# Kernel optimization log

Hardware: AMD Instinct MI355X
Metric: run time of the kernel (lower is better)

## Reference

```python
import jax, jax.numpy as jnp
import numpy as np

B, T, S, H = 16, 1024, 2048, 1024


def setup_inputs() -> dict:
    key = jax.random.key(0)
    k1, k2, k3, k4, k5 = jax.random.split(key, 5)
    output = jax.random.normal(k1, (B, T, H), dtype=jnp.float32)
    context = jax.random.normal(k2, (B, S, H), dtype=jnp.float32)
    # nn.Linear(H, H, bias=False): weight [H, H], y = x @ W.T
    attn_weight = jax.random.normal(k3, (H, H), dtype=jnp.float32) * (1.0 / np.sqrt(H))
    # nn.Linear(2H, H): weight [H, 2H], bias [H]
    linear_out_w = jax.random.normal(k4, (H, 2 * H), dtype=jnp.float32) * (1.0 / np.sqrt(2 * H))
    linear_out_b = jax.random.normal(k5, (H,), dtype=jnp.float32) * 0.01
    return {"output": output, "context": context, "attn_weight": attn_weight,
            "linear_out_w": linear_out_w, "linear_out_b": linear_out_b}


def reference(output, context, attn_weight, linear_out_w, linear_out_b):
    # weighted query projection (use_weight=True)
    q = jnp.einsum('bth,oh->bto', output, attn_weight)  # [B,T,H]
    # scores + softmax over encoder positions
    attn = jax.nn.softmax(jnp.einsum('bth,bsh->bts', q, context), axis=-1)  # [B,T,S]
    mix = jnp.einsum('bts,bsh->bth', attn, context)  # [B,T,H]
    comb = jnp.concatenate([mix, q], axis=-1)  # [B,T,2H]
    out = jnp.tanh(jnp.einsum('btk,hk->bth', comb, linear_out_w) + linear_out_b)
    return (out, attn)
```

## Files before the change

kernel.cpp:

```cpp
#include <hip/hip_runtime.h>
#include <math.h>

typedef short bf16x8 __attribute__((ext_vector_type(8)));
typedef float f32x4 __attribute__((ext_vector_type(4)));
typedef unsigned short u16;

#define AS1 __attribute__((address_space(1)))
#define AS3 __attribute__((address_space(3)))

constexpr int kB = 16, kT = 1024, kS = 2048, kH = 1024;
constexpr long NTH = (long)kB * kT * kH;
constexpr long NSH = (long)kB * kS * kH;

__device__ __forceinline__ u16 bf16_rne(float x) {
    unsigned u = __float_as_uint(x);
    u += 0x7FFFu + ((u >> 16) & 1u);
    return (u16)(u >> 16);
}
__device__ __forceinline__ float bf16_f32(u16 h) {
    return __uint_as_float(((unsigned)h) << 16);
}
__device__ __forceinline__ void split2(float x, u16& hi, u16& lo) {
    hi = bf16_rne(x);
    lo = bf16_rne(x - bf16_f32(hi));
}


__device__ __forceinline__ void stage_mat(const u16* __restrict__ g, long ld,
                                          u16* lds, int t, int wave) {
#pragma unroll
    for (int c = 0; c < 4; ++c) {
        int u = c * 512 + t;
        int r = u >> 3, j = u & 7;
        const u16* src = g + (long)r * ld + ((j ^ (r & 7)) << 3);
        u16* dst = lds + c * 4096 + wave * 512;
        __builtin_amdgcn_global_load_lds((AS1 void*)src, (AS3 void*)dst, 16, 0, 0);
    }
}

__device__ __forceinline__ void tile_compute(const u16* As, const u16* Bs,
                                             f32x4 acc[8][4], int wr, int wc,
                                             int l15, int cbu0, int cbu1) {
    bf16x8 b[4][2];
#pragma unroll
    for (int j = 0; j < 4; ++j) {
        const u16* base = Bs + (wc * 64 + j * 16 + l15) * 64;
        b[j][0] = *(const bf16x8*)(base + cbu0);
        b[j][1] = *(const bf16x8*)(base + cbu1);
    }
#pragma unroll
    for (int qm = 0; qm < 2; ++qm) {
        bf16x8 a[4][2];
#pragma unroll
        for (int i = 0; i < 4; ++i) {
            const u16* base = As + (wr * 128 + qm * 64 + i * 16 + l15) * 64;
            a[i][0] = *(const bf16x8*)(base + cbu0);
            a[i][1] = *(const bf16x8*)(base + cbu1);
        }
        __builtin_amdgcn_s_setprio(1);
#pragma unroll
        for (int i = 0; i < 4; ++i)
#pragma unroll
            for (int j = 0; j < 4; ++j) {
                acc[qm * 4 + i][j] = __builtin_amdgcn_mfma_f32_16x16x32_bf16(
                    a[i][0], b[j][0], acc[qm * 4 + i][j], 0, 0, 0);
                acc[qm * 4 + i][j] = __builtin_amdgcn_mfma_f32_16x16x32_bf16(
                    a[i][1], b[j][1], acc[qm * 4 + i][j], 0, 0, 0);
            }
        __builtin_amdgcn_s_setprio(0);
    }
}

#define WAIT_VM(N)                                            \
    asm volatile("s_waitcnt vmcnt(" #N ")" ::: "memory");     \
    __builtin_amdgcn_s_barrier();                             \
    __builtin_amdgcn_sched_barrier(0);

#define POST_BARRIER()                                        \
    __builtin_amdgcn_sched_barrier(0);                        \
    __builtin_amdgcn_s_barrier();                             \
    __builtin_amdgcn_sched_barrier(0);

template <int NT, int TPS>
__device__ __forceinline__ void gemm_core(const u16* a0, const u16* a1, const u16* a2,
                                          long lda,
                                          const u16* b0, const u16* b1, const u16* b2,
                                          long ldb, f32x4 acc[8][4]) {
    __shared__ u16 As[2][256 * 64], Bs[2][256 * 64];
    const int t = threadIdx.x, lane = t & 63, wave = t >> 6;
    const int wr = wave >> 2, wc = wave & 3, l15 = lane & 15, quad = lane >> 4;
    const int swzb = (l15 & 7) << 4;
    const int cbu0 = ((quad * 16) ^ swzb) >> 1;
    const int cbu1 = ((quad * 16 + 64) ^ swzb) >> 1;

    auto srcA = [&](int kt) {
        int seg = kt / TPS;
        const u16* p = (seg == 0) ? a0 : (seg == 1 ? a1 : a2);
        return p + (long)(kt % TPS) * 64;
    };
    auto srcB = [&](int kt) {
        int seg = kt / TPS;
        const u16* p = (seg == 0) ? b0 : (seg == 1 ? b1 : b2);
        return p + (long)(kt % TPS) * 64;
    };

    stage_mat(srcA(0), lda, As[0], t, wave);
    stage_mat(srcB(0), ldb, Bs[0], t, wave);
    __builtin_amdgcn_sched_barrier(0);
    stage_mat(srcA(1), lda, As[1], t, wave);
    stage_mat(srcB(1), ldb, Bs[1], t, wave);
    __builtin_amdgcn_sched_barrier(0);

#pragma unroll 1
    for (int it = 0; it < NT / 2 - 1; ++it) {
        int kt = 2 * it;
        WAIT_VM(8)
        tile_compute(As[0], Bs[0], acc, wr, wc, l15, cbu0, cbu1);
        POST_BARRIER()
        stage_mat(srcA(kt + 2), lda, As[0], t, wave);
        stage_mat(srcB(kt + 2), ldb, Bs[0], t, wave);

        WAIT_VM(8)
        tile_compute(As[1], Bs[1], acc, wr, wc, l15, cbu0, cbu1);
        POST_BARRIER()
        stage_mat(srcA(kt + 3), lda, As[1], t, wave);
        stage_mat(srcB(kt + 3), ldb, Bs[1], t, wave);
    }
    WAIT_VM(8)
    tile_compute(As[0], Bs[0], acc, wr, wc, l15, cbu0, cbu1);
    WAIT_VM(0)
    tile_compute(As[1], Bs[1], acc, wr, wc, l15, cbu0, cbu1);
}

__global__ __launch_bounds__(512, 2) void k_gemm_q(const u16* __restrict__ oh,
                                                   const u16* __restrict__ ol,
                                                   const u16* __restrict__ awh,
                                                   const u16* __restrict__ awl,
                                                   u16* __restrict__ Qhi,
                                                   u16* __restrict__ Qlo) {
    const long bm = (long)blockIdx.y * 256, bn = (long)blockIdx.x * 256;
    f32x4 acc[8][4] = {};
    gemm_core<48, 16>(oh + bm * kH, ol + bm * kH, oh + bm * kH, kH,
                      awh + bn * kH, awh + bn * kH, awl + bn * kH, kH, acc);
    const int t = threadIdx.x, lane = t & 63, wave = t >> 6;
    const int wr = wave >> 2, wc = wave & 3, l15 = lane & 15, quad = lane >> 4;
#pragma unroll
    for (int i = 0; i < 8; ++i)
#pragma unroll
        for (int j = 0; j < 4; ++j)
#pragma unroll
            for (int r = 0; r < 4; ++r) {
                long m = bm + wr * 128 + i * 16 + quad * 4 + r;
                long n = bn + wc * 64 + j * 16 + l15;
                float v = acc[i][j][r];
                u16 h = bf16_rne(v);
                Qhi[m * kH + n] = h;
                Qlo[m * kH + n] = bf16_rne(v - bf16_f32(h));
            }
}

__global__ __launch_bounds__(512, 2) void k_gemm_logits(const u16* __restrict__ Qh,
                                                        const u16* __restrict__ Ql,
                                                        const u16* __restrict__ Ch,
                                                        const u16* __restrict__ Cl,
                                                        float* __restrict__ Cout) {
    const int l = blockIdx.x;
    const int xcd = l & 7, slot = l >> 3;
    const int z = xcd + ((slot >> 5) << 3);
    const int inner = slot & 31;
    const long bn = (long)(inner & 7) * 256;
    const long bm = (long)(inner >> 3) * 256;
    const u16* qh = Qh + (long)z * kT * kH + bm * kH;
    const u16* ql = Ql + (long)z * kT * kH + bm * kH;
    const u16* ch = Ch + (long)z * kS * kH + bn * kH;
    const u16* cl = Cl + (long)z * kS * kH + bn * kH;
    f32x4 acc[8][4] = {};
    gemm_core<48, 16>(qh, ql, qh, kH, ch, ch, cl, kH, acc);
    float* C = Cout + (long)z * kT * kS;
    const int t = threadIdx.x, lane = t & 63, wave = t >> 6;
    const int wr = wave >> 2, wc = wave & 3, l15 = lane & 15, quad = lane >> 4;
#pragma unroll
    for (int i = 0; i < 8; ++i)
#pragma unroll
        for (int j = 0; j < 4; ++j)
#pragma unroll
            for (int r = 0; r < 4; ++r) {
                long m = bm + wr * 128 + i * 16 + quad * 4 + r;
                long n = bn + wc * 64 + j * 16 + l15;
                C[m * kS + n] = acc[i][j][r];
            }
}

__global__ __launch_bounds__(512, 2) void k_gemm_mix(const u16* __restrict__ attnb,
                                                     const u16* __restrict__ ctxT,
                                                     u16* __restrict__ Mixb) {
    const int l = blockIdx.x;
    const int xcd = l & 7, slot = l >> 3;
    const int z = xcd + ((slot >> 4) << 3);
    const int inner = slot & 15;
    const long bn = (long)(inner & 3) * 256;
    const long bm = (long)(inner >> 2) * 256;
    const u16* Ab = attnb + (long)z * kT * kS + bm * kS;
    const u16* Bb = ctxT + (long)z * kH * kS + bn * kS;
    f32x4 acc[8][4] = {};
    gemm_core<32, 32>(Ab, Ab, Ab, kS, Bb, Bb, Bb, kS, acc);
    u16* C = Mixb + (long)z * kT * kH;
    const int t = threadIdx.x, lane = t & 63, wave = t >> 6;
    const int wr = wave >> 2, wc = wave & 3, l15 = lane & 15, quad = lane >> 4;
#pragma unroll
    for (int i = 0; i < 8; ++i)
#pragma unroll
        for (int j = 0; j < 4; ++j)
#pragma unroll
            for (int r = 0; r < 4; ++r) {
                long m = bm + wr * 128 + i * 16 + quad * 4 + r;
                long n = bn + wc * 64 + j * 16 + l15;
                C[m * kH + n] = bf16_rne(acc[i][j][r]);
            }
}

__global__ __launch_bounds__(512, 2) void k_gemm_out(const u16* __restrict__ mixc,
                                                     const u16* __restrict__ qc,
                                                     const u16* __restrict__ lwb,
                                                     const float* __restrict__ bias,
                                                     float* __restrict__ Out) {
    const long bm = (long)blockIdx.y * 256, bn = (long)blockIdx.x * 256;
    f32x4 acc[8][4] = {};
    gemm_core<32, 16>(mixc + bm * kH, qc + bm * kH, qc + bm * kH, kH,
                      lwb + bn * 2 * kH, lwb + bn * 2 * kH + kH, lwb + bn * 2 * kH + kH,
                      2 * kH, acc);
    const int t = threadIdx.x, lane = t & 63, wave = t >> 6;
    const int wr = wave >> 2, wc = wave & 3, l15 = lane & 15, quad = lane >> 4;
#pragma unroll
    for (int j = 0; j < 4; ++j) {
        long n = bn + wc * 64 + j * 16 + l15;
        float bj = bias[n];
#pragma unroll
        for (int i = 0; i < 8; ++i)
#pragma unroll
            for (int r = 0; r < 4; ++r) {
                long m = bm + wr * 128 + i * 16 + quad * 4 + r;
                Out[m * kH + n] = tanhf(acc[i][j][r] + bj);
            }
    }
}

__global__ __launch_bounds__(256) void split_f32(const float* __restrict__ src,
                                                 u16* __restrict__ hi, u16* __restrict__ lo,
                                                 long n4) {
    for (long i = (long)blockIdx.x * 256 + threadIdx.x; i < n4; i += (long)gridDim.x * 256) {
        float4 v = ((const float4*)src)[i];
        u16 h0, l0, h1, l1, h2, l2, h3, l3;
        split2(v.x, h0, l0); split2(v.y, h1, l1);
        split2(v.z, h2, l2); split2(v.w, h3, l3);
        ((ushort4*)hi)[i] = make_ushort4(h0, h1, h2, h3);
        ((ushort4*)lo)[i] = make_ushort4(l0, l1, l2, l3);
    }
}

__global__ __launch_bounds__(256) void cvt_f32(const float* __restrict__ src,
                                               u16* __restrict__ dst, long n4) {
    for (long i = (long)blockIdx.x * 256 + threadIdx.x; i < n4; i += (long)gridDim.x * 256) {
        float4 v = ((const float4*)src)[i];
        ((ushort4*)dst)[i] = make_ushort4(bf16_rne(v.x), bf16_rne(v.y),
                                          bf16_rne(v.z), bf16_rne(v.w));
    }
}

__global__ __launch_bounds__(256) void copy16(const uint4* __restrict__ src,
                                              uint4* __restrict__ dst, long n) {
    for (long i = (long)blockIdx.x * 256 + threadIdx.x; i < n; i += (long)gridDim.x * 256)
        dst[i] = src[i];
}

__global__ __launch_bounds__(256) void transpose_bf16(const u16* __restrict__ in,
                                                      u16* __restrict__ outp) {
    __shared__ u16 tile[64 * 72];
    const int t = threadIdx.x;
    const u16* src = in + (long)blockIdx.z * kS * kH + (long)(blockIdx.y * 64) * kH
                     + blockIdx.x * 64;
#pragma unroll
    for (int it = 0; it < 2; ++it) {
        int idx = it * 256 + t;
        int s = idx >> 3, hc = (idx & 7) << 3;
        uint4 v = *(const uint4*)(src + (long)s * kH + hc);
        const u16* pv = (const u16*)&v;
#pragma unroll
        for (int k = 0; k < 8; ++k) tile[(hc + k) * 72 + s] = pv[k];
    }
    __syncthreads();
    u16* dst = outp + (long)blockIdx.z * kH * kS + (long)(blockIdx.x * 64) * kS
               + blockIdx.y * 64;
#pragma unroll
    for (int it = 0; it < 2; ++it) {
        int idx = it * 256 + t;
        int h = idx >> 3, sc = (idx & 7) << 3;
        *(uint4*)(dst + (long)h * kS + sc) = *(const uint4*)&tile[h * 72 + sc];
    }
}

__global__ __launch_bounds__(256) void softmax_rows(float* __restrict__ P,
                                                    u16* __restrict__ Pb) {
    __shared__ float red[4];
    float* p = P + (long)blockIdx.x * kS;
    u16* pb = Pb + (long)blockIdx.x * kS;
    const int t = threadIdx.x;

    float4 v0 = ((const float4*)p)[t];
    float4 v1 = ((const float4*)p)[t + 256];

    float m = fmaxf(fmaxf(fmaxf(v0.x, v0.y), fmaxf(v0.z, v0.w)),
                    fmaxf(fmaxf(v1.x, v1.y), fmaxf(v1.z, v1.w)));
#pragma unroll
    for (int o = 32; o > 0; o >>= 1) m = fmaxf(m, __shfl_xor(m, o));
    if ((t & 63) == 0) red[t >> 6] = m;
    __syncthreads();
    m = fmaxf(fmaxf(red[0], red[1]), fmaxf(red[2], red[3]));
    __syncthreads();

    v0.x = expf(v0.x - m); v0.y = expf(v0.y - m);
    v0.z = expf(v0.z - m); v0.w = expf(v0.w - m);
    v1.x = expf(v1.x - m); v1.y = expf(v1.y - m);
    v1.z = expf(v1.z - m); v1.w = expf(v1.w - m);

    float s = v0.x + v0.y + v0.z + v0.w + v1.x + v1.y + v1.z + v1.w;
#pragma unroll
    for (int o = 32; o > 0; o >>= 1) s += __shfl_xor(s, o);
    if ((t & 63) == 0) red[t >> 6] = s;
    __syncthreads();
    s = red[0] + red[1] + red[2] + red[3];

    const float inv = 1.0f / s;
    v0.x *= inv; v0.y *= inv; v0.z *= inv; v0.w *= inv;
    v1.x *= inv; v1.y *= inv; v1.z *= inv; v1.w *= inv;

    ((float4*)p)[t]       = v0;
    ((float4*)p)[t + 256] = v1;
    ((ushort4*)pb)[t]       = make_ushort4(bf16_rne(v0.x), bf16_rne(v0.y),
                                           bf16_rne(v0.z), bf16_rne(v0.w));
    ((ushort4*)pb)[t + 256] = make_ushort4(bf16_rne(v1.x), bf16_rne(v1.y),
                                           bf16_rne(v1.z), bf16_rne(v1.w));
}

extern "C" void kernel_launch(void* const* d_in, const int* in_sizes, int n_in,
                              void* d_out, int out_size, void* d_ws, size_t ws_size,
                              hipStream_t stream) {
    (void)in_sizes; (void)n_in; (void)out_size; (void)ws_size;

    const float* outp = (const float*)d_in[0];
    const float* ctx  = (const float*)d_in[1];
    const float* aw   = (const float*)d_in[2];
    const float* lw   = (const float*)d_in[3];
    const float* lb   = (const float*)d_in[4];

    float* out  = (float*)d_out;
    float* attn = out + NTH;

    u16* ws = (u16*)d_ws;
    u16* ctx_hi = ws;
    u16* ctx_lo = ws + NSH;
    u16* q_hi = (u16*)out;
    u16* q_lo = q_hi + NTH;
    u16* oh  = (u16*)attn;
    u16* ol  = oh + NTH;
    u16* awh = ol + NTH;
    u16* awl = awh + (long)kH * kH;
    u16* ctxT  = ws + NSH;
    u16* attnb = ws;
    u16* mixb  = q_lo;
    u16* q_c   = ws;
    u16* mix_c = ws + NTH;
    u16* lwb   = ws + 2 * NTH;

    split_f32<<<2048, 256, 0, stream>>>(ctx, ctx_hi, ctx_lo, NSH / 4);
    split_f32<<<2048, 256, 0, stream>>>(outp, oh, ol, NTH / 4);
    split_f32<<<1024, 256, 0, stream>>>(aw, awh, awl, (long)kH * kH / 4);

    k_gemm_q<<<dim3(kH / 256, (kB * kT) / 256), 512, 0, stream>>>(oh, ol, awh, awl,
                                                                  q_hi, q_lo);
    k_gemm_logits<<<512, 512, 0, stream>>>(q_hi, q_lo, ctx_hi, ctx_lo, attn);

    transpose_bf16<<<dim3(kH / 64, kS / 64, kB), 256, 0, stream>>>(ctx_hi, ctxT);
    softmax_rows<<<kB * kT, 256, 0, stream>>>(attn, attnb);

    k_gemm_mix<<<256, 512, 0, stream>>>(attnb, ctxT, mixb);

    copy16<<<2048, 256, 0, stream>>>((const uint4*)q_hi, (uint4*)ws, (2 * NTH) / 8);
    cvt_f32<<<2048, 256, 0, stream>>>(lw, lwb, (long)kH * 2 * kH / 4);

    k_gemm_out<<<dim3(kH / 256, (kB * kT) / 256), 512, 0, stream>>>(mix_c, q_c, lwb, lb, out);
}
```

Baseline: 891.3 us.

## Restructure GEMM main loop into four-phase interleaved load/MFMA schedule

Replaces the two-stage double-buffered GEMM loop with a four-phase schedule per K tile. Each phase issues half-tile global-to-LDS loads for the next A tile or for the B tile two steps ahead, then runs a 16-MFMA quadrant under raised priority, with barriers between phases. The aim is to spread memory traffic across the compute and keep the matrix units busier than whole-tile staging followed by bulk compute allows. It adds more barriers per tile and clamped, redundant loads past the last tile.

```diff
diff --git a/kernel.cpp b/kernel.cpp
--- a/kernel.cpp
+++ b/kernel.cpp
@@ -26,60 +26,17 @@
 }
 
 
-__device__ __forceinline__ void stage_mat(const u16* __restrict__ g, long ld,
-                                          u16* lds, int t, int wave) {
-#pragma unroll
-    for (int c = 0; c < 4; ++c) {
-        int u = c * 512 + t;
-        int r = u >> 3, j = u & 7;
-        const u16* src = g + (long)r * ld + ((j ^ (r & 7)) << 3);
-        u16* dst = lds + c * 4096 + wave * 512;
-        __builtin_amdgcn_global_load_lds((AS1 void*)src, (AS3 void*)dst, 16, 0, 0);
-    }
-}
-
-__device__ __forceinline__ void tile_compute(const u16* As, const u16* Bs,
-                                             f32x4 acc[8][4], int wr, int wc,
-                                             int l15, int cbu0, int cbu1) {
-    bf16x8 b[4][2];
-#pragma unroll
-    for (int j = 0; j < 4; ++j) {
-        const u16* base = Bs + (wc * 64 + j * 16 + l15) * 64;
-        b[j][0] = *(const bf16x8*)(base + cbu0);
-        b[j][1] = *(const bf16x8*)(base + cbu1);
-    }
-#pragma unroll
-    for (int qm = 0; qm < 2; ++qm) {
-        bf16x8 a[4][2];
-#pragma unroll
-        for (int i = 0; i < 4; ++i) {
-            const u16* base = As + (wr * 128 + qm * 64 + i * 16 + l15) * 64;
-            a[i][0] = *(const bf16x8*)(base + cbu0);
-            a[i][1] = *(const bf16x8*)(base + cbu1);
-        }
-        __builtin_amdgcn_s_setprio(1);
-#pragma unroll
-        for (int i = 0; i < 4; ++i)
-#pragma unroll
-            for (int j = 0; j < 4; ++j) {
-                acc[qm * 4 + i][j] = __builtin_amdgcn_mfma_f32_16x16x32_bf16(
-                    a[i][0], b[j][0], acc[qm * 4 + i][j], 0, 0, 0);
-                acc[qm * 4 + i][j] = __builtin_amdgcn_mfma_f32_16x16x32_bf16(
-                    a[i][1], b[j][1], acc[qm * 4 + i][j], 0, 0, 0);
-            }
-        __builtin_amdgcn_s_setprio(0);
-    }
-}
-
-#define WAIT_VM(N)                                            \
-    asm volatile("s_waitcnt vmcnt(" #N ")" ::: "memory");     \
-    __builtin_amdgcn_s_barrier();                             \
-    __builtin_amdgcn_sched_barrier(0);
-
-#define POST_BARRIER()                                        \
-    __builtin_amdgcn_sched_barrier(0);                        \
-    __builtin_amdgcn_s_barrier();                             \
-    __builtin_amdgcn_sched_barrier(0);
+#define PHASE_PRE()                                          \
+    __builtin_amdgcn_sched_barrier(0);                       \
+    __builtin_amdgcn_s_barrier();                            \
+    asm volatile("s_waitcnt lgkmcnt(0)" ::: "memory");       \
+    __builtin_amdgcn_sched_barrier(0);                       \
+    __builtin_amdgcn_s_setprio(1);
+
+#define PHASE_POST()                                         \
+    __builtin_amdgcn_s_setprio(0);                           \
+    __builtin_amdgcn_sched_barrier(0);                       \
+    __builtin_amdgcn_s_barrier();
 
 template <int NT, int TPS>
 __device__ __forceinline__ void gemm_core(const u16* a0, const u16* a1, const u16* a2,
@@ -103,33 +60,107 @@
         const u16* p = (seg == 0) ? b0 : (seg == 1 ? b1 : b2);
         return p + (long)(kt % TPS) * 64;
     };
-
-    stage_mat(srcA(0), lda, As[0], t, wave);
-    stage_mat(srcB(0), ldb, Bs[0], t, wave);
-    __builtin_amdgcn_sched_barrier(0);
-    stage_mat(srcA(1), lda, As[1], t, wave);
-    stage_mat(srcB(1), ldb, Bs[1], t, wave);
-    __builtin_amdgcn_sched_barrier(0);
+    auto stageA = [&](int kt, int h, int buf) {
+        const u16* g = srcA(kt < NT ? kt : NT - 1) + (long)h * 128 * lda;
+        u16* region = &As[buf][h * 8192];
+#pragma unroll
+        for (int c = 0; c < 2; ++c) {
+            int u = c * 512 + t;
+            int r = u >> 3, j8 = u & 7;
+            const u16* src = g + (long)r * lda + ((j8 ^ (r & 7)) << 3);
+            u16* dst = region + c * 4096 + wave * 512;
+            __builtin_amdgcn_global_load_lds((AS1 void*)src, (AS3 void*)dst, 16, 0, 0);
+        }
+    };
+    auto stageB = [&](int kt, int h, int buf) {
+        const u16* g = srcB(kt < NT ? kt : NT - 1) + (long)h * 128 * ldb;
+        u16* region = &Bs[buf][h * 8192];
+#pragma unroll
+        for (int c = 0; c < 2; ++c) {
+            int u = c * 512 + t;
+            int r = u >> 3, j8 = u & 7;
+            const u16* src = g + (long)r * ldb + ((j8 ^ (r & 7)) << 3);
+            u16* dst = region + c * 4096 + wave * 512;
+            __builtin_amdgcn_global_load_lds((AS1 void*)src, (AS3 void*)dst, 16, 0, 0);
+        }
+    };
+
+    stageB(0, 0, 0); __builtin_amdgcn_sched_barrier(0);
+    stageB(0, 1, 0); __builtin_amdgcn_sched_barrier(0);
+    stageA(0, 0, 0); __builtin_amdgcn_sched_barrier(0);
+    stageA(0, 1, 0); __builtin_amdgcn_sched_barrier(0);
+    stageB(1, 0, 1); __builtin_amdgcn_sched_barrier(0);
+    stageB(1, 1, 1); __builtin_amdgcn_sched_barrier(0);
+    asm volatile("s_waitcnt vmcnt(4)" ::: "memory");
+    __builtin_amdgcn_s_barrier();
 
 #pragma unroll 1
-    for (int it = 0; it < NT / 2 - 1; ++it) {
-        int kt = 2 * it;
-        WAIT_VM(8)
-        tile_compute(As[0], Bs[0], acc, wr, wc, l15, cbu0, cbu1);
-        POST_BARRIER()
-        stage_mat(srcA(kt + 2), lda, As[0], t, wave);
-        stage_mat(srcB(kt + 2), ldb, Bs[0], t, wave);
-
-        WAIT_VM(8)
-        tile_compute(As[1], Bs[1], acc, wr, wc, l15, cbu0, cbu1);
-        POST_BARRIER()
-        stage_mat(srcA(kt + 3), lda, As[1], t, wave);
-        stage_mat(srcB(kt + 3), ldb, Bs[1], t, wave);
-    }
-    WAIT_VM(8)
-    tile_compute(As[0], Bs[0], acc, wr, wc, l15, cbu0, cbu1);
-    WAIT_VM(0)
-    tile_compute(As[1], Bs[1], acc, wr, wc, l15, cbu0, cbu1);
+    for (int j = 0; j < NT; ++j) {
+        const int c = j & 1;
+        bf16x8 a[4][2], bA[2][2], bB[2][2];
+
+        auto mfma16 = [&](bf16x8 (&a4)[4][2], bf16x8 (&b2)[2][2], int ih, int jh) {
+#pragma unroll
+            for (int i2 = 0; i2 < 4; ++i2)
+#pragma unroll
+                for (int j2 = 0; j2 < 2; ++j2) {
+                    acc[ih * 4 + i2][jh * 2 + j2] = __builtin_amdgcn_mfma_f32_16x16x32_bf16(
+                        a4[i2][0], b2[j2][0], acc[ih * 4 + i2][jh * 2 + j2], 0, 0, 0);
+                    acc[ih * 4 + i2][jh * 2 + j2] = __builtin_amdgcn_mfma_f32_16x16x32_bf16(
+                        a4[i2][1], b2[j2][1], acc[ih * 4 + i2][jh * 2 + j2], 0, 0, 0);
+                }
+        };
+
+#pragma unroll
+        for (int i = 0; i < 4; ++i) {
+            const u16* base = &As[c][(wr * 128 + i * 16 + l15) * 64];
+            a[i][0] = *(const bf16x8*)(base + cbu0);
+            a[i][1] = *(const bf16x8*)(base + cbu1);
+        }
+#pragma unroll
+        for (int jj = 0; jj < 2; ++jj) {
+            const u16* base = &Bs[c][(wc * 64 + jj * 16 + l15) * 64];
+            bA[jj][0] = *(const bf16x8*)(base + cbu0);
+            bA[jj][1] = *(const bf16x8*)(base + cbu1);
+        }
+        stageA(j + 1, 0, c ^ 1);
+        PHASE_PRE()
+        mfma16(a, bA, 0, 0);
+        PHASE_POST()
+
+#pragma unroll
+        for (int jj = 0; jj < 2; ++jj) {
+            const u16* base = &Bs[c][(wc * 64 + (2 + jj) * 16 + l15) * 64];
+            bB[jj][0] = *(const bf16x8*)(base + cbu0);
+            bB[jj][1] = *(const bf16x8*)(base + cbu1);
+        }
+        stageA(j + 1, 1, c ^ 1);
+        PHASE_PRE()
+        mfma16(a, bB, 0, 1);
+        PHASE_POST()
+
+#pragma unroll
+        for (int i = 0; i < 4; ++i) {
+            const u16* base = &As[c][(wr * 128 + (4 + i) * 16 + l15) * 64];
+            a[i][0] = *(const bf16x8*)(base + cbu0);
+            a[i][1] = *(const bf16x8*)(base + cbu1);
+        }
+        stageB(j + 2, 0, c);
+        PHASE_PRE()
+        mfma16(a, bA, 1, 0);
+        PHASE_POST()
+
+        stageB(j + 2, 1, c);
+        __builtin_amdgcn_sched_barrier(0);
+        __builtin_amdgcn_s_barrier();
+        __builtin_amdgcn_s_setprio(1);
+        mfma16(a, bB, 1, 1);
+        __builtin_amdgcn_s_setprio(0);
+        __builtin_amdgcn_sched_barrier(0);
+        asm volatile("s_waitcnt vmcnt(4)" ::: "memory");
+        __builtin_amdgcn_s_barrier();
+    }
+    asm volatile("s_waitcnt vmcnt(0)" ::: "memory");
 }
 
 __global__ __launch_bounds__(512, 2) void k_gemm_q(const u16* __restrict__ oh,
```

Measured after the change: 980.5 us. +10.0%, slower.

## Add K-split half-tile pipelined GEMM core for the logits kernel

Applied to the files above, without the earlier changes.

Adds a new GEMM mainloop that stages each 64-wide K tile as two 32-wide halves into double-buffered LDS. Each half gets its own vmcnt wait and barrier, and the next tile's half is loaded while the current half is computed. MFMA issue is bracketed with setprio. Only the logits GEMM uses it. The aim is finer-grained overlap of global-to-LDS loads with MFMA compute, at the cost of twice as many barriers per tile and a different LDS swizzle.

```diff
diff --git a/kernel.cpp b/kernel.cpp
--- a/kernel.cpp
+++ b/kernel.cpp
@@ -24,7 +24,6 @@
     hi = bf16_rne(x);
     lo = bf16_rne(x - bf16_f32(hi));
 }
-
 
 __device__ __forceinline__ void stage_mat(const u16* __restrict__ g, long ld,
                                           u16* lds, int t, int wave) {
@@ -130,6 +129,76 @@
     tile_compute(As[0], Bs[0], acc, wr, wc, l15, cbu0, cbu1);
     WAIT_VM(0)
     tile_compute(As[1], Bs[1], acc, wr, wc, l15, cbu0, cbu1);
+}
+
+template <int NT, int TPS>
+__device__ __forceinline__ void gemm_core_ks(const u16* a0, const u16* a1, const u16* a2,
+                                             long lda,
+                                             const u16* b0, const u16* b1, const u16* b2,
+                                             long ldb, f32x4 acc[8][4]) {
+    __shared__ u16 As[2][2][256 * 32], Bs[2][2][256 * 32];
+    const int t = threadIdx.x, lane = t & 63, wave = t >> 6;
+    const int wr = wave >> 2, wc = wave & 3, l15 = lane & 15, quad = lane >> 4;
+    const int cu = (quad ^ ((l15 >> 1) & 3)) << 3;
+
+    auto srcA = [&](int kt) {
+        int seg = kt / TPS;
+        const u16* p = (seg == 0) ? a0 : (seg == 1 ? a1 : a2);
+        return p + (long)(kt % TPS) * 64;
+    };
+    auto srcB = [&](int kt) {
+        int seg = kt / TPS;
+        const u16* p = (seg == 0) ? b0 : (seg == 1 ? b1 : b2);
+        return p + (long)(kt % TPS) * 64;
+    };
+    auto stageH = [&](const u16* g, long ld, int kh, u16* region) {
+        const u16* gh = g + kh * 32;
+#pragma unroll
+        for (int c = 0; c < 2; ++c) {
+            int u = c * 512 + t;
+            int r = u >> 2, c16 = u & 3;
+            const u16* src = gh + (long)r * ld + ((c16 ^ ((r >> 1) & 3)) << 3);
+            u16* dst = region + c * 4096 + wave * 512;
+            __builtin_amdgcn_global_load_lds((AS1 void*)src, (AS3 void*)dst, 16, 0, 0);
+        }
+    };
+
+    stageH(srcA(0), lda, 0, As[0][0]);
+    stageH(srcB(0), ldb, 0, Bs[0][0]);
+    __builtin_amdgcn_sched_barrier(0);
+    stageH(srcA(0), lda, 1, As[0][1]);
+    stageH(srcB(0), ldb, 1, Bs[0][1]);
+    __builtin_amdgcn_sched_barrier(0);
+
+#pragma unroll 1
+    for (int j = 0; j < NT; ++j) {
+        const int buf = j & 1;
+        const int skt = (j + 1 < NT) ? j + 1 : NT - 1;
+#pragma unroll
+        for (int kh = 0; kh < 2; ++kh) {
+            asm volatile("s_waitcnt vmcnt(4)" ::: "memory");
+            __builtin_amdgcn_s_barrier();
+            __builtin_amdgcn_sched_barrier(0);
+            stageH(srcA(skt), lda, kh, As[buf ^ 1][kh]);
+            stageH(srcB(skt), ldb, kh, Bs[buf ^ 1][kh]);
+            bf16x8 a[8], b[4];
+#pragma unroll
+            for (int i = 0; i < 8; ++i)
+                a[i] = *(const bf16x8*)(&As[buf][kh][(wr * 128 + i * 16 + l15) * 32 + cu]);
+#pragma unroll
+            for (int jj = 0; jj < 4; ++jj)
+                b[jj] = *(const bf16x8*)(&Bs[buf][kh][(wc * 64 + jj * 16 + l15) * 32 + cu]);
+            __builtin_amdgcn_s_setprio(1);
+#pragma unroll
+            for (int i = 0; i < 8; ++i)
+#pragma unroll
+                for (int jj = 0; jj < 4; ++jj)
+                    acc[i][jj] = __builtin_amdgcn_mfma_f32_16x16x32_bf16(
+                        a[i], b[jj], acc[i][jj], 0, 0, 0);
+            __builtin_amdgcn_s_setprio(0);
+        }
+    }
+    asm volatile("s_waitcnt vmcnt(0)" ::: "memory");
 }
 
 __global__ __launch_bounds__(512, 2) void k_gemm_q(const u16* __restrict__ oh,
@@ -175,7 +244,7 @@
     const u16* ch = Ch + (long)z * kS * kH + bn * kH;
     const u16* cl = Cl + (long)z * kS * kH + bn * kH;
     f32x4 acc[8][4] = {};
-    gemm_core<48, 16>(qh, ql, qh, kH, ch, ch, cl, kH, acc);
+    gemm_core_ks<48, 16>(qh, ql, qh, kH, ch, ch, cl, kH, acc);
     float* C = Cout + (long)z * kT * kS;
     const int t = threadIdx.x, lane = t & 63, wave = t >> 6;
     const int wr = wave >> 2, wc = wave & 3, l15 = lane & 15, quad = lane >> 4;
```

Measured after the change: 925.1 us. 3.8% more time.

## Use four-phase interleaved load/MFMA pipeline for logits GEMM

Applied to the files above, without the earlier changes.

Adds a new GEMM core for the logits kernel that splits each K-tile into four MFMA phases. Half-tile global-to-LDS loads are interleaved between the phases, with barriers and setprio around each MFMA cluster. It stages B two tiles ahead and A one tile ahead, so memory traffic overlaps with compute more finely than the old two-buffer loop. The cost is more barriers per tile and more complex buffer-reuse ordering, which could introduce races or stalls.

```diff
diff --git a/kernel.cpp b/kernel.cpp
--- a/kernel.cpp
+++ b/kernel.cpp
@@ -24,7 +24,6 @@
     hi = bf16_rne(x);
     lo = bf16_rne(x - bf16_f32(hi));
 }
-
 
 __device__ __forceinline__ void stage_mat(const u16* __restrict__ g, long ld,
                                           u16* lds, int t, int wave) {
@@ -130,6 +129,148 @@
     tile_compute(As[0], Bs[0], acc, wr, wc, l15, cbu0, cbu1);
     WAIT_VM(0)
     tile_compute(As[1], Bs[1], acc, wr, wc, l15, cbu0, cbu1);
+}
+
+template <int NT, int TPS>
+__device__ __forceinline__ void gemm_core_p4(const u16* a0p, const u16* a1p,
+                                             const u16* a2p, long lda,
+                                             const u16* b0p, const u16* b1p,
+                                             const u16* b2p, long ldb, f32x4 acc[8][4]) {
+    __shared__ u16 As[2][256 * 64], Bs[2][256 * 64];
+    const int t = threadIdx.x, lane = t & 63, wave = t >> 6;
+    const int wr = wave >> 2, wc = wave & 3, l15 = lane & 15, quad = lane >> 4;
+    const int swzb = (l15 & 7) << 4;
+    const int cbu0 = ((quad * 16) ^ swzb) >> 1;
+    const int cbu1 = ((quad * 16 + 64) ^ swzb) >> 1;
+
+    auto srcA = [&](int kt) {
+        int seg = kt / TPS;
+        const u16* p = (seg == 0) ? a0p : (seg == 1 ? a1p : a2p);
+        return p + (long)(kt % TPS) * 64;
+    };
+    auto srcB = [&](int kt) {
+        int seg = kt / TPS;
+        const u16* p = (seg == 0) ? b0p : (seg == 1 ? b1p : b2p);
+        return p + (long)(kt % TPS) * 64;
+    };
+    auto stageH = [&](const u16* g, long ld, int h, u16* bufbase) {
+        const u16* gh = g + (long)h * 128 * ld;
+        u16* region = bufbase + h * 8192;
+#pragma unroll
+        for (int cc = 0; cc < 2; ++cc) {
+            int u = cc * 512 + t;
+            int r = u >> 3, j8 = u & 7;
+            const u16* src = gh + (long)r * ld + ((j8 ^ (r & 7)) << 3);
+            u16* dst = region + cc * 4096 + wave * 512;
+            __builtin_amdgcn_global_load_lds((AS1 void*)src, (AS3 void*)dst, 16, 0, 0);
+        }
+    };
+
+    stageH(srcA(0), lda, 0, As[0]);
+    stageH(srcA(0), lda, 1, As[0]);
+    stageH(srcB(0), ldb, 0, Bs[0]);
+    stageH(srcB(0), ldb, 1, Bs[0]);
+    stageH(srcB(1), ldb, 0, Bs[1]);
+    stageH(srcB(1), ldb, 1, Bs[1]);
+    asm volatile("s_waitcnt vmcnt(4)" ::: "memory");
+    __builtin_amdgcn_s_barrier();
+
+#pragma unroll 1
+    for (int j = 0; j < NT; ++j) {
+        const int c = j & 1;
+        const int jA = (j + 1 < NT) ? j + 1 : NT - 1;
+        const int jB = (j + 2 < NT) ? j + 2 : NT - 1;
+        const u16* As_c = As[c];
+        const u16* Bs_c = Bs[c];
+        bf16x8 aF[8][2], bF[4][2];
+
+#pragma unroll
+        for (int n = 0; n < 4; ++n) {
+            const u16* base = Bs_c + (wc * 64 + n * 16 + l15) * 64;
+            bF[n][0] = *(const bf16x8*)(base + cbu0);
+            bF[n][1] = *(const bf16x8*)(base + cbu1);
+        }
+#pragma unroll
+        for (int i = 0; i < 4; ++i) {
+            const u16* base = As_c + (wr * 128 + i * 16 + l15) * 64;
+            aF[i][0] = *(const bf16x8*)(base + cbu0);
+            aF[i][1] = *(const bf16x8*)(base + cbu1);
+        }
+        stageH(srcA(jA), lda, 0, As[c ^ 1]);
+        __builtin_amdgcn_s_barrier();
+        asm volatile("s_waitcnt lgkmcnt(0)" ::: "memory");
+        __builtin_amdgcn_sched_barrier(0);
+        __builtin_amdgcn_s_setprio(1);
+#pragma unroll
+        for (int i = 0; i < 4; ++i)
+#pragma unroll
+            for (int n = 0; n < 2; ++n) {
+                acc[i][n] = __builtin_amdgcn_mfma_f32_16x16x32_bf16(
+                    aF[i][0], bF[n][0], acc[i][n], 0, 0, 0);
+                acc[i][n] = __builtin_amdgcn_mfma_f32_16x16x32_bf16(
+                    aF[i][1], bF[n][1], acc[i][n], 0, 0, 0);
+            }
+        __builtin_amdgcn_s_setprio(0);
+        __builtin_amdgcn_sched_barrier(0);
+        __builtin_amdgcn_s_barrier();
+
+#pragma unroll
+        for (int i = 0; i < 4; ++i) {
+            const u16* base = As_c + (wr * 128 + 64 + i * 16 + l15) * 64;
+            aF[4 + i][0] = *(const bf16x8*)(base + cbu0);
+            aF[4 + i][1] = *(const bf16x8*)(base + cbu1);
+        }
+        stageH(srcA(jA), lda, 1, As[c ^ 1]);
+        __builtin_amdgcn_s_barrier();
+        asm volatile("s_waitcnt lgkmcnt(0)" ::: "memory");
+        __builtin_amdgcn_sched_barrier(0);
+        __builtin_amdgcn_s_setprio(1);
+#pragma unroll
+        for (int i = 0; i < 4; ++i)
+#pragma unroll
+            for (int n = 0; n < 2; ++n) {
+                acc[i][2 + n] = __builtin_amdgcn_mfma_f32_16x16x32_bf16(
+                    aF[i][0], bF[2 + n][0], acc[i][2 + n], 0, 0, 0);
+                acc[i][2 + n] = __builtin_amdgcn_mfma_f32_16x16x32_bf16(
+                    aF[i][1], bF[2 + n][1], acc[i][2 + n], 0, 0, 0);
+            }
+        __builtin_amdgcn_s_setprio(0);
+        __builtin_amdgcn_sched_barrier(0);
+        __builtin_amdgcn_s_barrier();
+
+        stageH(srcB(jB), ldb, 0, Bs[c]);
+        __builtin_amdgcn_s_barrier();
+        __builtin_amdgcn_s_setprio(1);
+#pragma unroll
+        for (int i = 0; i < 4; ++i)
+#pragma unroll
+            for (int n = 0; n < 2; ++n) {
+                acc[4 + i][n] = __builtin_amdgcn_mfma_f32_16x16x32_bf16(
+                    aF[4 + i][0], bF[n][0], acc[4 + i][n], 0, 0, 0);
+                acc[4 + i][n] = __builtin_amdgcn_mfma_f32_16x16x32_bf16(
+                    aF[4 + i][1], bF[n][1], acc[4 + i][n], 0, 0, 0);
+            }
+        __builtin_amdgcn_s_setprio(0);
+        __builtin_amdgcn_sched_barrier(0);
+        __builtin_amdgcn_s_barrier();
+
+        stageH(srcB(jB), ldb, 1, Bs[c]);
+        __builtin_amdgcn_s_barrier();
+        __builtin_amdgcn_s_setprio(1);
+#pragma unroll
+        for (int i = 0; i < 4; ++i)
+#pragma unroll
+            for (int n = 0; n < 2; ++n) {
+                acc[4 + i][2 + n] = __builtin_amdgcn_mfma_f32_16x16x32_bf16(
+                    aF[4 + i][0], bF[2 + n][0], acc[4 + i][2 + n], 0, 0, 0);
+                acc[4 + i][2 + n] = __builtin_amdgcn_mfma_f32_16x16x32_bf16(
+                    aF[4 + i][1], bF[2 + n][1], acc[4 + i][2 + n], 0, 0, 0);
+            }
+        __builtin_amdgcn_s_setprio(0);
+        __builtin_amdgcn_sched_barrier(0);
+        asm volatile("s_waitcnt vmcnt(4)" ::: "memory");
+        __builtin_amdgcn_s_barrier();
+    }
 }
 
 __global__ __launch_bounds__(512, 2) void k_gemm_q(const u16* __restrict__ oh,
@@ -175,7 +316,7 @@
     const u16* ch = Ch + (long)z * kS * kH + bn * kH;
     const u16* cl = Cl + (long)z * kS * kH + bn * kH;
     f32x4 acc[8][4] = {};
-    gemm_core<48, 16>(qh, ql, qh, kH, ch, ch, cl, kH, acc);
+    gemm_core_p4<48, 16>(qh, ql, qh, kH, ch, ch, cl, kH, acc);
     float* C = Cout + (long)z * kT * kS;
     const int t = threadIdx.x, lane = t & 63, wave = t >> 6;
     const int wr = wave >> 2, wc = wave & 3, l15 = lane & 15, quad = lane >> 4;
```

Measured after the change: 935.1 us. +4.9%, slower.
